# Kernel optimization log

Hardware: AMD Instinct MI355X
Metric: run time of the kernel (lower is better)

Reference implementation:

```python
import jax, jax.numpy as jnp
import numpy as np

N_NODES = 50000
N_EDGES = 800000
D_IN = 128
D_HID = 128


def _sage_conv(x, src, dst, W_l, b_l, W_r, num_nodes):
    # PyG SAGEConv (mean aggr): out = lin_l(mean_{j in N(i)} x_j) + lin_r(x_i)
    msgs = x[src]  # [E, d] irregular gather
    agg = jax.ops.segment_sum(msgs, dst, num_segments=num_nodes)  # [N, d]
    cnt = jax.ops.segment_sum(jnp.ones((dst.shape[0], 1), x.dtype), dst, num_segments=num_nodes)
    agg = agg / jnp.maximum(cnt, 1.0)  # mean over in-neighbors
    return agg @ W_l.T + b_l + x @ W_r.T


def setup_inputs() -> dict:
    key = jax.random.key(0)
    ks = jax.random.split(key, 8)
    x = jax.random.normal(ks[0], (N_NODES, D_IN), dtype=jnp.float32)
    edge_index = jax.random.randint(ks[1], (2, N_EDGES), 0, N_NODES, dtype=jnp.int64)
    s0 = 1.0 / np.sqrt(D_IN)
    s1 = 1.0 / np.sqrt(D_HID)
    return {
        "x": x,
        "edge_index": edge_index,
        "W_l0": jax.random.uniform(ks[2], (D_HID, D_IN), jnp.float32, -s0, s0),
        "b_l0": jnp.zeros((D_HID,), jnp.float32),
        "W_r0": jax.random.uniform(ks[3], (D_HID, D_IN), jnp.float32, -s0, s0),
        "W_l1": jax.random.uniform(ks[4], (D_HID, D_HID), jnp.float32, -s1, s1),
        "b_l1": jnp.zeros((D_HID,), jnp.float32),
        "W_r1": jax.random.uniform(ks[5], (D_HID, D_HID), jnp.float32, -s1, s1),
    }


def reference(x, edge_index, W_l0, b_l0, W_r0, W_l1, b_l1, W_r1):
    src, dst = edge_index[0], edge_index[1]
    n = x.shape[0]
    # layer 0 + ReLU (dropout is identity at inference)
    h = _sage_conv(x, src, dst, W_l0, b_l0, W_r0, n)
    h = jax.nn.relu(h)
    # layer 1 (no activation on last layer)
    out = _sage_conv(h, src, dst, W_l1, b_l1, W_r1, n)
    return out
```

## Files before the change

kernel.cpp:

```cpp
#include <hip/hip_runtime.h>


typedef __attribute__((ext_vector_type(8))) short short8;
typedef __attribute__((ext_vector_type(4))) float f32x4;

#define DEV __device__ __forceinline__

DEV unsigned short f2b(float f) {
  unsigned u = __builtin_bit_cast(unsigned, f);
  u += 0x7fffu + ((u >> 16) & 1u);
  return (unsigned short)(u >> 16);
}
DEV float b2f(unsigned short h) {
  unsigned u = ((unsigned)h) << 16;
  return __builtin_bit_cast(float, u);
}

constexpr int N_NODES = 50000;
constexpr int N_EDGES = 800000;
constexpr int D = 128;
constexpr int NBUCK = (N_NODES + 255) / 256;
constexpr int BCAP = 5120;
constexpr int EPB = (N_EDGES + NBUCK - 1) / NBUCK;

__global__ __launch_bounds__(256) void bin_kernel(const int* __restrict__ src,
                                                  const int* __restrict__ dst,
                                                  int* __restrict__ g_bcnt,
                                                  unsigned* __restrict__ staging) {
  __shared__ int cnt[NBUCK];
  __shared__ int cur[NBUCK];
  int t = threadIdx.x;
  for (int i = t; i < NBUCK; i += 256) cnt[i] = 0;
  __syncthreads();
  int beg = blockIdx.x * EPB;
  int end = min(beg + EPB, N_EDGES);
  for (int e = beg + t; e < end; e += 256) {
    atomicAdd(&cnt[dst[e] >> 8], 1);
  }
  __syncthreads();
  for (int i = t; i < NBUCK; i += 256) {
    cur[i] = atomicAdd(&g_bcnt[i], cnt[i]);
  }
  __syncthreads();
  for (int e = beg + t; e < end; e += 256) {
    int d = dst[e];
    int b = d >> 8;
    int p = atomicAdd(&cur[b], 1);
    if (p >= BCAP) p = BCAP - 1;
    staging[b * BCAP + p] = ((unsigned)(d & 255) << 16) | (unsigned)src[e];
  }
}

__global__ void scan_buck(const int* __restrict__ g_bcnt, int* __restrict__ g_bbase,
                          int* __restrict__ offs) {
  __shared__ int tmp[256];
  int t = threadIdx.x;
  int v = (t < NBUCK) ? g_bcnt[t] : 0;
  tmp[t] = v;
  __syncthreads();
  for (int off = 1; off < 256; off <<= 1) {
    int u = (t >= off) ? tmp[t - off] : 0;
    __syncthreads();
    tmp[t] += u;
    __syncthreads();
  }
  if (t < NBUCK) g_bbase[t] = tmp[t] - v;
  if (t == 0) offs[N_NODES] = N_EDGES;
}

__global__ __launch_bounds__(256) void fill2_kernel(const unsigned* __restrict__ staging,
                                                    const int* __restrict__ g_bcnt,
                                                    const int* __restrict__ g_bbase,
                                                    int* __restrict__ offs,
                                                    int* __restrict__ csr) {
  __shared__ int hist[256];
  __shared__ int tmp[256];
  __shared__ int cur[256];
  int b = blockIdx.x;
  int t = threadIdx.x;
  int n = g_bcnt[b];
  int bb = g_bbase[b];
  const unsigned* st = staging + b * BCAP;
  hist[t] = 0;
  __syncthreads();
  for (int e = t; e < n; e += 256) atomicAdd(&hist[st[e] >> 16], 1);
  __syncthreads();
  int v = hist[t];
  tmp[t] = v;
  __syncthreads();
  for (int off = 1; off < 256; off <<= 1) {
    int u = (t >= off) ? tmp[t - off] : 0;
    __syncthreads();
    tmp[t] += u;
    __syncthreads();
  }
  int excl = tmp[t] - v;
  int node = b * 256 + t;
  if (node < N_NODES) offs[node] = bb + excl;
  cur[t] = bb + excl;
  __syncthreads();
  for (int e = t; e < n; e += 256) {
    unsigned pk = st[e];
    int p = atomicAdd(&cur[pk >> 16], 1);
    csr[p] = (int)(pk & 0xffffu);
  }
}

__global__ void convert_kernel(const float* __restrict__ in, unsigned short* __restrict__ out) {
  int i = blockIdx.x * blockDim.x + threadIdx.x;
  const int n4 = N_NODES * D / 4;
  if (i >= n4) return;
  f32x4 v = ((const f32x4*)in)[i];
  uint2 o;
  o.x = (unsigned)f2b(v.x) | ((unsigned)f2b(v.y) << 16);
  o.y = (unsigned)f2b(v.z) | ((unsigned)f2b(v.w) << 16);
  ((uint2*)out)[i] = o;
}

__global__ void prep_weights(const float* __restrict__ Wl0, const float* __restrict__ Wr0,
                             const float* __restrict__ Wl1, const float* __restrict__ Wr1,
                             unsigned short* __restrict__ Bf) {
  int f = blockIdx.x * blockDim.x + threadIdx.x;
  if (f >= 2 * 32 * 128) return;
  int layer = f >> 12;
  int kchunk = (f >> 7) & 31;
  int n = f & 127;
  const float* W;
  if (layer == 0) W = (kchunk < 16) ? Wl0 : Wr0;
  else            W = (kchunk < 16) ? Wl1 : Wr1;
  int k = (kchunk & 15) * 8;
  const f32x4* row = (const f32x4*)(W + n * D + k);
  f32x4 a = row[0], b = row[1];
  uint2 lo, hi;
  lo.x = (unsigned)f2b(a.x) | ((unsigned)f2b(a.y) << 16);
  lo.y = (unsigned)f2b(a.z) | ((unsigned)f2b(a.w) << 16);
  hi.x = (unsigned)f2b(b.x) | ((unsigned)f2b(b.y) << 16);
  hi.y = (unsigned)f2b(b.z) | ((unsigned)f2b(b.w) << 16);
  uint4 pk = {lo.x, lo.y, hi.x, hi.y};
  *(uint4*)(Bf + (size_t)f * 8) = pk;
}

__global__ void agg_kernel(const unsigned short* __restrict__ feat,
                           const int* __restrict__ csr_src,
                           const int* __restrict__ offs,
                           unsigned short* __restrict__ out) {
  int w = (int)((blockIdx.x * blockDim.x + threadIdx.x) >> 6);
  int lane = threadIdx.x & 63;
  if (w >= N_NODES) return;
  int s = offs[w], e = offs[w + 1];
  const unsigned* f = (const unsigned*)feat;
  float ax = 0.f, ay = 0.f;
  int k = s;
  for (; k + 4 <= e; k += 4) {
    int s0 = csr_src[k], s1 = csr_src[k + 1], s2 = csr_src[k + 2], s3 = csr_src[k + 3];
    unsigned u0 = f[s0 * 64 + lane];
    unsigned u1 = f[s1 * 64 + lane];
    unsigned u2 = f[s2 * 64 + lane];
    unsigned u3 = f[s3 * 64 + lane];
    ax += b2f((unsigned short)u0) + b2f((unsigned short)u1) +
          b2f((unsigned short)u2) + b2f((unsigned short)u3);
    ay += b2f((unsigned short)(u0 >> 16)) + b2f((unsigned short)(u1 >> 16)) +
          b2f((unsigned short)(u2 >> 16)) + b2f((unsigned short)(u3 >> 16));
  }
  for (; k < e; ++k) {
    unsigned u = f[csr_src[k] * 64 + lane];
    ax += b2f((unsigned short)u);
    ay += b2f((unsigned short)(u >> 16));
  }
  float inv = 1.0f / (float)max(e - s, 1);
  unsigned o = (unsigned)f2b(ax * inv) | ((unsigned)f2b(ay * inv) << 16);
  ((unsigned*)out)[w * 64 + lane] = o;
}

__global__ __launch_bounds__(256) void gemm_kernel(
    const unsigned short* __restrict__ Aagg,
    const unsigned short* __restrict__ Afeat,
    const unsigned short* __restrict__ Bf,
    const float* __restrict__ bias,
    float* __restrict__ out_f32,
    unsigned short* __restrict__ out_bf16,
    int relu_bf16) {
  int wave = threadIdx.x >> 6;
  int lane = threadIdx.x & 63;
  int ml = lane & 15;
  int quad = lane >> 4;
  int node0 = blockIdx.x * 64 + wave * 16;

  int arow = node0 + ml;
  if (arow >= N_NODES) arow = N_NODES - 1;

  f32x4 acc[8];
#pragma unroll
  for (int t = 0; t < 8; ++t) acc[t] = (f32x4){0.f, 0.f, 0.f, 0.f};

  const short8* bf8 = (const short8*)Bf;
#pragma unroll
  for (int mat = 0; mat < 2; ++mat) {
    const unsigned short* A = mat ? Afeat : Aagg;
    const short8* arow8 = (const short8*)(A + (size_t)arow * D);
    int kbase = mat * 16;
#pragma unroll
    for (int kc = 0; kc < 4; ++kc) {
      short8 af = arow8[kc * 4 + quad];
      int kchunk = kbase + kc * 4 + quad;
      const short8* brow = bf8 + kchunk * 128;
#pragma unroll
      for (int nt = 0; nt < 8; ++nt) {
        short8 bfr = brow[nt * 16 + ml];
        acc[nt] = __builtin_amdgcn_mfma_f32_16x16x32_bf16(af, bfr, acc[nt], 0, 0, 0);
      }
    }
  }

#pragma unroll
  for (int nt = 0; nt < 8; ++nt) {
    int col = nt * 16 + ml;
    float bv = bias[col];
#pragma unroll
    for (int r = 0; r < 4; ++r) {
      int node = node0 + quad * 4 + r;
      if (node >= N_NODES) continue;
      float v = acc[nt][r] + bv;
      if (relu_bf16) {
        v = v > 0.f ? v : 0.f;
        out_bf16[(size_t)node * D + col] = f2b(v);
      } else {
        out_f32[(size_t)node * D + col] = v;
      }
    }
  }
}

extern "C" void kernel_launch(void* const* d_in, const int* in_sizes, int n_in,
                              void* d_out, int out_size, void* d_ws, size_t ws_size,
                              hipStream_t stream) {
  const float* x   = (const float*)d_in[0];
  const int*   ei  = (const int*)d_in[1];
  const float* Wl0 = (const float*)d_in[2];
  const float* bl0 = (const float*)d_in[3];
  const float* Wr0 = (const float*)d_in[4];
  const float* Wl1 = (const float*)d_in[5];
  const float* bl1 = (const float*)d_in[6];
  const float* Wr1 = (const float*)d_in[7];
  float* out = (float*)d_out;

  char* ws = (char*)d_ws;
  size_t o = 0;
  auto carve = [&](size_t bytes) {
    char* p = ws + o;
    o += bytes;
    o = (o + 255) & ~(size_t)255;
    return p;
  };
  int* offs       = (int*)carve((size_t)(N_NODES + 1) * 4);
  int* csr        = (int*)carve((size_t)N_EDGES * 4);
  int* g_bcnt     = (int*)carve((size_t)NBUCK * 4);
  int* g_bbase    = (int*)carve((size_t)NBUCK * 4);
  unsigned* staging = (unsigned*)carve((size_t)NBUCK * BCAP * 4);
  unsigned short* Bf   = (unsigned short*)carve((size_t)2 * 32 * 128 * 8 * 2);
  unsigned short* xb   = (unsigned short*)carve((size_t)N_NODES * D * 2);
  unsigned short* aggb = (unsigned short*)carve((size_t)N_NODES * D * 2);
  unsigned short* hb   = (unsigned short*)carve((size_t)N_NODES * D * 2);

  const int* srcp = ei;
  const int* dstp = ei + N_EDGES;

  hipMemsetAsync(g_bcnt, 0, (size_t)NBUCK * 4, stream);
  bin_kernel<<<NBUCK, 256, 0, stream>>>(srcp, dstp, g_bcnt, staging);
  scan_buck<<<1, 256, 0, stream>>>(g_bcnt, g_bbase, offs);
  fill2_kernel<<<NBUCK, 256, 0, stream>>>(staging, g_bcnt, g_bbase, offs, csr);
  convert_kernel<<<(N_NODES * D / 4 + 255) / 256, 256, 0, stream>>>(x, xb);
  prep_weights<<<(2 * 32 * 128 + 255) / 256, 256, 0, stream>>>(Wl0, Wr0, Wl1, Wr1, Bf);

  const int GEMM_BLOCKS = (N_NODES + 63) / 64;
  agg_kernel<<<(N_NODES + 3) / 4, 256, 0, stream>>>(xb, csr, offs, aggb);
  gemm_kernel<<<GEMM_BLOCKS, 256, 0, stream>>>(aggb, xb, Bf, bl0, nullptr, hb, 1);
  agg_kernel<<<(N_NODES + 3) / 4, 256, 0, stream>>>(hb, csr, offs, aggb);
  gemm_kernel<<<GEMM_BLOCKS, 256, 0, stream>>>(aggb, hb, Bf + 32 * 128 * 8, bl1,
                                               out, nullptr, 0);
}
```

Baseline: 235.9 us.

## Merge setup kernels, fold bucket scan into fill, double GEMM rows per wave

Combines the bf16 conversion of x, the weight packing and the edge binning into one heterogeneous launch that dispatches on block index. The single-block bucket scan is dropped: every fill block recomputes the prefix over bucket counts itself. The GEMM now has each wave handle two 16-row tiles, so each B fragment load feeds two MFMAs and half as many blocks are launched. The intent is to cut launch and serialization overhead and B-operand traffic, at the cost of redundant scans per block and more accumulator registers.

```diff
diff --git a/kernel.cpp b/kernel.cpp
--- a/kernel.cpp
+++ b/kernel.cpp
@@ -22,17 +22,54 @@
 constexpr int NBUCK = (N_NODES + 255) / 256;
 constexpr int BCAP = 5120;
 constexpr int EPB = (N_EDGES + NBUCK - 1) / NBUCK;
-
-__global__ __launch_bounds__(256) void bin_kernel(const int* __restrict__ src,
-                                                  const int* __restrict__ dst,
-                                                  int* __restrict__ g_bcnt,
-                                                  unsigned* __restrict__ staging) {
+constexpr int NCONV = (N_NODES * D / 4) / 256;
+constexpr int NPREP = (2 * 32 * 128) / 256;
+
+__global__ __launch_bounds__(256) void setup_kernel(
+    const float* __restrict__ x, unsigned short* __restrict__ xb,
+    const float* __restrict__ Wl0, const float* __restrict__ Wr0,
+    const float* __restrict__ Wl1, const float* __restrict__ Wr1,
+    unsigned short* __restrict__ Bf,
+    const int* __restrict__ src, const int* __restrict__ dst,
+    int* __restrict__ g_bcnt, unsigned* __restrict__ staging) {
   __shared__ int cnt[NBUCK];
   __shared__ int cur[NBUCK];
+  int bid = blockIdx.x;
   int t = threadIdx.x;
+
+  if (bid < NCONV) {
+    int i = bid * 256 + t;
+    f32x4 v = ((const f32x4*)x)[i];
+    uint2 o;
+    o.x = (unsigned)f2b(v.x) | ((unsigned)f2b(v.y) << 16);
+    o.y = (unsigned)f2b(v.z) | ((unsigned)f2b(v.w) << 16);
+    ((uint2*)xb)[i] = o;
+    return;
+  }
+  if (bid < NCONV + NPREP) {
+    int f = (bid - NCONV) * 256 + t;
+    int layer = f >> 12;
+    int kchunk = (f >> 7) & 31;
+    int n = f & 127;
+    const float* W;
+    if (layer == 0) W = (kchunk < 16) ? Wl0 : Wr0;
+    else            W = (kchunk < 16) ? Wl1 : Wr1;
+    int k = (kchunk & 15) * 8;
+    const f32x4* row = (const f32x4*)(W + n * D + k);
+    f32x4 a = row[0], b = row[1];
+    uint4 pk;
+    pk.x = (unsigned)f2b(a.x) | ((unsigned)f2b(a.y) << 16);
+    pk.y = (unsigned)f2b(a.z) | ((unsigned)f2b(a.w) << 16);
+    pk.z = (unsigned)f2b(b.x) | ((unsigned)f2b(b.y) << 16);
+    pk.w = (unsigned)f2b(b.z) | ((unsigned)f2b(b.w) << 16);
+    *(uint4*)(Bf + (size_t)f * 8) = pk;
+    return;
+  }
+
+  int blk = bid - NCONV - NPREP;
   for (int i = t; i < NBUCK; i += 256) cnt[i] = 0;
   __syncthreads();
-  int beg = blockIdx.x * EPB;
+  int beg = blk * EPB;
   int end = min(beg + EPB, N_EDGES);
   for (int e = beg + t; e < end; e += 256) {
     atomicAdd(&cnt[dst[e] >> 8], 1);
@@ -51,35 +88,30 @@
   }
 }
 
-__global__ void scan_buck(const int* __restrict__ g_bcnt, int* __restrict__ g_bbase,
-                          int* __restrict__ offs) {
-  __shared__ int tmp[256];
-  int t = threadIdx.x;
-  int v = (t < NBUCK) ? g_bcnt[t] : 0;
-  tmp[t] = v;
-  __syncthreads();
-  for (int off = 1; off < 256; off <<= 1) {
-    int u = (t >= off) ? tmp[t - off] : 0;
-    __syncthreads();
-    tmp[t] += u;
-    __syncthreads();
-  }
-  if (t < NBUCK) g_bbase[t] = tmp[t] - v;
-  if (t == 0) offs[N_NODES] = N_EDGES;
-}
-
 __global__ __launch_bounds__(256) void fill2_kernel(const unsigned* __restrict__ staging,
                                                     const int* __restrict__ g_bcnt,
-                                                    const int* __restrict__ g_bbase,
                                                     int* __restrict__ offs,
                                                     int* __restrict__ csr) {
+  __shared__ int cnts[256];
+  __shared__ int tmp[256];
   __shared__ int hist[256];
-  __shared__ int tmp[256];
   __shared__ int cur[256];
   int b = blockIdx.x;
   int t = threadIdx.x;
-  int n = g_bcnt[b];
-  int bb = g_bbase[b];
+  int c = (t < NBUCK) ? g_bcnt[t] : 0;
+  cnts[t] = c;
+  tmp[t] = c;
+  __syncthreads();
+  for (int off = 1; off < 256; off <<= 1) {
+    int u = (t >= off) ? tmp[t - off] : 0;
+    __syncthreads();
+    tmp[t] += u;
+    __syncthreads();
+  }
+  int n = cnts[b];
+  int bb = tmp[b] - n;
+  if (b == 0 && t == 0) offs[N_NODES] = N_EDGES;
+
   const unsigned* st = staging + b * BCAP;
   hist[t] = 0;
   __syncthreads();
@@ -104,40 +136,6 @@
     int p = atomicAdd(&cur[pk >> 16], 1);
     csr[p] = (int)(pk & 0xffffu);
   }
-}
-
-__global__ void convert_kernel(const float* __restrict__ in, unsigned short* __restrict__ out) {
-  int i = blockIdx.x * blockDim.x + threadIdx.x;
-  const int n4 = N_NODES * D / 4;
-  if (i >= n4) return;
-  f32x4 v = ((const f32x4*)in)[i];
-  uint2 o;
-  o.x = (unsigned)f2b(v.x) | ((unsigned)f2b(v.y) << 16);
-  o.y = (unsigned)f2b(v.z) | ((unsigned)f2b(v.w) << 16);
-  ((uint2*)out)[i] = o;
-}
-
-__global__ void prep_weights(const float* __restrict__ Wl0, const float* __restrict__ Wr0,
-                             const float* __restrict__ Wl1, const float* __restrict__ Wr1,
-                             unsigned short* __restrict__ Bf) {
-  int f = blockIdx.x * blockDim.x + threadIdx.x;
-  if (f >= 2 * 32 * 128) return;
-  int layer = f >> 12;
-  int kchunk = (f >> 7) & 31;
-  int n = f & 127;
-  const float* W;
-  if (layer == 0) W = (kchunk < 16) ? Wl0 : Wr0;
-  else            W = (kchunk < 16) ? Wl1 : Wr1;
-  int k = (kchunk & 15) * 8;
-  const f32x4* row = (const f32x4*)(W + n * D + k);
-  f32x4 a = row[0], b = row[1];
-  uint2 lo, hi;
-  lo.x = (unsigned)f2b(a.x) | ((unsigned)f2b(a.y) << 16);
-  lo.y = (unsigned)f2b(a.z) | ((unsigned)f2b(a.w) << 16);
-  hi.x = (unsigned)f2b(b.x) | ((unsigned)f2b(b.y) << 16);
-  hi.y = (unsigned)f2b(b.z) | ((unsigned)f2b(b.w) << 16);
-  uint4 pk = {lo.x, lo.y, hi.x, hi.y};
-  *(uint4*)(Bf + (size_t)f * 8) = pk;
 }
 
 __global__ void agg_kernel(const unsigned short* __restrict__ feat,
@@ -184,48 +182,55 @@
   int lane = threadIdx.x & 63;
   int ml = lane & 15;
   int quad = lane >> 4;
-  int node0 = blockIdx.x * 64 + wave * 16;
-
-  int arow = node0 + ml;
-  if (arow >= N_NODES) arow = N_NODES - 1;
-
-  f32x4 acc[8];
-#pragma unroll
-  for (int t = 0; t < 8; ++t) acc[t] = (f32x4){0.f, 0.f, 0.f, 0.f};
+  int node0 = blockIdx.x * 128 + wave * 32;
+
+  int ar0 = node0 + ml;       if (ar0 >= N_NODES) ar0 = N_NODES - 1;
+  int ar1 = node0 + 16 + ml;  if (ar1 >= N_NODES) ar1 = N_NODES - 1;
+
+  f32x4 acc[2][8];
+#pragma unroll
+  for (int m = 0; m < 2; ++m)
+#pragma unroll
+    for (int t = 0; t < 8; ++t) acc[m][t] = (f32x4){0.f, 0.f, 0.f, 0.f};
 
   const short8* bf8 = (const short8*)Bf;
 #pragma unroll
   for (int mat = 0; mat < 2; ++mat) {
     const unsigned short* A = mat ? Afeat : Aagg;
-    const short8* arow8 = (const short8*)(A + (size_t)arow * D);
+    const short8* a0 = (const short8*)(A + (size_t)ar0 * D);
+    const short8* a1 = (const short8*)(A + (size_t)ar1 * D);
     int kbase = mat * 16;
 #pragma unroll
     for (int kc = 0; kc < 4; ++kc) {
-      short8 af = arow8[kc * 4 + quad];
-      int kchunk = kbase + kc * 4 + quad;
-      const short8* brow = bf8 + kchunk * 128;
+      short8 af0 = a0[kc * 4 + quad];
+      short8 af1 = a1[kc * 4 + quad];
+      const short8* brow = bf8 + (kbase + kc * 4 + quad) * 128;
 #pragma unroll
       for (int nt = 0; nt < 8; ++nt) {
         short8 bfr = brow[nt * 16 + ml];
-        acc[nt] = __builtin_amdgcn_mfma_f32_16x16x32_bf16(af, bfr, acc[nt], 0, 0, 0);
+        acc[0][nt] = __builtin_amdgcn_mfma_f32_16x16x32_bf16(af0, bfr, acc[0][nt], 0, 0, 0);
+        acc[1][nt] = __builtin_amdgcn_mfma_f32_16x16x32_bf16(af1, bfr, acc[1][nt], 0, 0, 0);
       }
     }
   }
 
 #pragma unroll
-  for (int nt = 0; nt < 8; ++nt) {
-    int col = nt * 16 + ml;
-    float bv = bias[col];
-#pragma unroll
-    for (int r = 0; r < 4; ++r) {
-      int node = node0 + quad * 4 + r;
-      if (node >= N_NODES) continue;
-      float v = acc[nt][r] + bv;
-      if (relu_bf16) {
-        v = v > 0.f ? v : 0.f;
-        out_bf16[(size_t)node * D + col] = f2b(v);
-      } else {
-        out_f32[(size_t)node * D + col] = v;
+  for (int tile = 0; tile < 2; ++tile) {
+#pragma unroll
+    for (int nt = 0; nt < 8; ++nt) {
+      int col = nt * 16 + ml;
+      float bv = bias[col];
+#pragma unroll
+      for (int r = 0; r < 4; ++r) {
+        int node = node0 + tile * 16 + quad * 4 + r;
+        if (node >= N_NODES) continue;
+        float v = acc[tile][nt][r] + bv;
+        if (relu_bf16) {
+          v = v > 0.f ? v : 0.f;
+          out_bf16[(size_t)node * D + col] = f2b(v);
+        } else {
+          out_f32[(size_t)node * D + col] = v;
+        }
       }
     }
   }
@@ -255,7 +260,6 @@
   int* offs       = (int*)carve((size_t)(N_NODES + 1) * 4);
   int* csr        = (int*)carve((size_t)N_EDGES * 4);
   int* g_bcnt     = (int*)carve((size_t)NBUCK * 4);
-  int* g_bbase    = (int*)carve((size_t)NBUCK * 4);
   unsigned* staging = (unsigned*)carve((size_t)NBUCK * BCAP * 4);
   unsigned short* Bf   = (unsigned short*)carve((size_t)2 * 32 * 128 * 8 * 2);
   unsigned short* xb   = (unsigned short*)carve((size_t)N_NODES * D * 2);
@@ -266,13 +270,11 @@
   const int* dstp = ei + N_EDGES;
 
   hipMemsetAsync(g_bcnt, 0, (size_t)NBUCK * 4, stream);
-  bin_kernel<<<NBUCK, 256, 0, stream>>>(srcp, dstp, g_bcnt, staging);
-  scan_buck<<<1, 256, 0, stream>>>(g_bcnt, g_bbase, offs);
-  fill2_kernel<<<NBUCK, 256, 0, stream>>>(staging, g_bcnt, g_bbase, offs, csr);
-  convert_kernel<<<(N_NODES * D / 4 + 255) / 256, 256, 0, stream>>>(x, xb);
-  prep_weights<<<(2 * 32 * 128 + 255) / 256, 256, 0, stream>>>(Wl0, Wr0, Wl1, Wr1, Bf);
-
-  const int GEMM_BLOCKS = (N_NODES + 63) / 64;
+  setup_kernel<<<NCONV + NPREP + NBUCK, 256, 0, stream>>>(
+      x, xb, Wl0, Wr0, Wl1, Wr1, Bf, srcp, dstp, g_bcnt, staging);
+  fill2_kernel<<<NBUCK, 256, 0, stream>>>(staging, g_bcnt, offs, csr);
+
+  const int GEMM_BLOCKS = (N_NODES + 127) / 128;
   agg_kernel<<<(N_NODES + 3) / 4, 256, 0, stream>>>(xb, csr, offs, aggb);
   gemm_kernel<<<GEMM_BLOCKS, 256, 0, stream>>>(aggb, xb, Bf, bl0, nullptr, hb, 1);
   agg_kernel<<<(N_NODES + 3) / 4, 256, 0, stream>>>(hb, csr, offs, aggb);
```

Measured after the change: 251.2 us. +6.5%, slower.
